# Kernel tuning notes

Hardware: AMD Instinct MI355X
Metric: run time of the kernel (lower is better)

## Reference

```python
import jax, jax.numpy as jnp
import numpy as np

NUM_LAYERS = 3
CHANNELS = 8
IN_CHANNELS = 8
MASK_FEAT_STRIDE = 8
MASK_OUT_STRIDE = 4
FACTOR = MASK_FEAT_STRIDE // MASK_OUT_STRIDE  # 2

# param split sizes (weights first, then biases), matching parse_dynamic_params
W0 = (IN_CHANNELS + 2) * CHANNELS  # 80
W1 = CHANNELS * CHANNELS           # 64
W2 = CHANNELS * 1                  # 8
B0 = CHANNELS
B1 = CHANNELS
B2 = 1
NUM_GEN_PARAMS = W0 + W1 + W2 + B0 + B1 + B2  # 169


def compute_locations(h, w, stride):
    # matches adet.utils.comm.compute_locations: centers of stride-cells, (x, y)
    sx = jnp.arange(w, dtype=jnp.float32) * stride + stride // 2
    sy = jnp.arange(h, dtype=jnp.float32) * stride + stride // 2
    yy, xx = jnp.meshgrid(sy, sx, indexing='ij')
    return jnp.stack([xx.reshape(-1), yy.reshape(-1)], axis=1)  # [H*W, 2]


def _interp_axis_align(x, out_size, axis):
    # 1D bilinear with align_corners=True along `axis`
    in_size = x.shape[axis]
    pos = jnp.arange(out_size, dtype=jnp.float32) * ((in_size - 1) / (out_size - 1))
    i0 = jnp.floor(pos).astype(jnp.int32)
    i1 = jnp.minimum(i0 + 1, in_size - 1)
    w1 = (pos - i0.astype(jnp.float32)).astype(x.dtype)
    shape = [1] * x.ndim
    shape[axis] = out_size
    w1 = w1.reshape(shape)
    x0 = jnp.take(x, i0, axis=axis)
    x1 = jnp.take(x, i1, axis=axis)
    return x0 * (1 - w1) + x1 * w1


def aligned_bilinear(t, factor):
    # matches adet.utils.comm.aligned_bilinear
    if factor == 1:
        return t
    h, w = t.shape[2], t.shape[3]
    t = jnp.pad(t, ((0, 0), (0, 0), (0, 1), (0, 1)), mode='edge')
    oh, ow = factor * h + 1, factor * w + 1
    t = _interp_axis_align(t, oh, 2)
    t = _interp_axis_align(t, ow, 3)
    pad = factor // 2
    t = jnp.pad(t, ((0, 0), (0, 0), (pad, 0), (pad, 0)), mode='edge')
    return t[:, :, :oh - 1, :ow - 1]  # [N, C, factor*h, factor*w]


def setup_inputs() -> dict:
    key = jax.random.key(0)
    k1, k2, k3, k4, k5 = jax.random.split(key, 5)
    N, H, W = 2, 128, 192
    n_inst = 128
    mask_feats = jax.random.normal(k1, (N, IN_CHANNELS, H, W), dtype=jnp.float32)
    mask_head_params = jax.random.normal(k2, (n_inst, NUM_GEN_PARAMS), dtype=jnp.float32) * 0.1
    instance_locations = jax.random.uniform(k3, (n_inst, 2), dtype=jnp.float32) * 1024.0
    sizes_of_interest = jnp.array([64.0, 128.0, 256.0, 512.0, 1e8, 2e8], dtype=jnp.float32)
    im_inds = jax.random.randint(k4, (n_inst,), 0, N, dtype=jnp.int32)
    fpn_levels = jax.random.randint(k5, (n_inst,), 0, 5, dtype=jnp.int32)
    return {
        'mask_feats': mask_feats,
        'mask_head_params': mask_head_params,
        'instance_locations': instance_locations,
        'sizes_of_interest': sizes_of_interest,
        'im_inds': im_inds,
        'fpn_levels': fpn_levels,
    }


def reference(mask_feats, mask_head_params, instance_locations, sizes_of_interest, im_inds, fpn_levels):
    N, C, H, W = mask_feats.shape
    n = mask_head_params.shape[0]
    HW = H * W

    locs = compute_locations(H, W, MASK_FEAT_STRIDE)                 # [HW, 2]
    rel = instance_locations[:, None, :] - locs[None, :, :]          # [n, HW, 2]
    rel = jnp.transpose(rel, (0, 2, 1))                              # [n, 2, HW]
    soi = sizes_of_interest[fpn_levels]                              # [n]
    rel = rel / soi[:, None, None]

    feats = mask_feats[im_inds].reshape(n, C, HW)                    # gather per-instance image feats
    x = jnp.concatenate([rel, feats], axis=1)                        # [n, C+2, HW]

    p = mask_head_params
    w0 = p[:, :W0].reshape(n, CHANNELS, IN_CHANNELS + 2)
    w1 = p[:, W0:W0 + W1].reshape(n, CHANNELS, CHANNELS)
    w2 = p[:, W0 + W1:W0 + W1 + W2].reshape(n, 1, CHANNELS)
    off = W0 + W1 + W2
    b0 = p[:, off:off + B0]
    b1 = p[:, off + B0:off + B0 + B1]
    b2 = p[:, off + B0 + B1:off + B0 + B1 + B2]

    # per-instance dynamic 1x1-conv MLP (grouped conv == batched matmul)
    x = jax.nn.relu(jnp.einsum('noi,nip->nop', w0, x) + b0[:, :, None])
    x = jax.nn.relu(jnp.einsum('noi,nip->nop', w1, x) + b1[:, :, None])
    x = jnp.einsum('noi,nip->nop', w2, x) + b2[:, :, None]           # [n, 1, HW]

    mask_logits = x.reshape(n, 1, H, W)
    return aligned_bilinear(mask_logits, FACTOR)                     # [n, 1, 2H, 2W]
```

## Files before the change

kernel.cpp:

```cpp
#include <hip/hip_runtime.h>
#include <hip/hip_bf16.h>

#define NUM_INST 128
#define H_ 128
#define W_ 192
#define HW_ (H_ * W_)
#define OH_ 256
#define OW_ 384
#define NPAR 169

typedef float v2f __attribute__((ext_vector_type(2)));

static __device__ __forceinline__ float bf2f(unsigned short u) {
    union { unsigned int i; float f; } v;
    v.i = ((unsigned int)u) << 16;
    return v.f;
}
static __device__ __forceinline__ float hi2f(unsigned int u) {
    union { unsigned int i; float f; } v;
    v.i = u & 0xFFFF0000u;
    return v.f;
}
static __device__ __forceinline__ float lo2f(unsigned int u) {
    union { unsigned int i; float f; } v;
    v.i = u << 16;
    return v.f;
}
static __device__ __forceinline__ unsigned int f2bf(float f) {
    unsigned int u = __float_as_uint(f);
    return (u + 0x7fffu + ((u >> 16) & 1u)) >> 16;
}
static __device__ __forceinline__ v2f pkfma(v2f a, v2f b, v2f c) {
    return __builtin_elementwise_fma(a, b, c);
}
static __device__ __forceinline__ v2f pkrelu(v2f a) {
    const v2f z = {0.0f, 0.0f};
    return __builtin_elementwise_max(a, z);
}

__global__ __launch_bounds__(256) void fused_maskhead(
    const void* __restrict__ mf_v,
    const void* __restrict__ par_v,
    const void* __restrict__ loc_v,
    const void* __restrict__ soi_v,
    const int*  __restrict__ im_inds,
    const int*  __restrict__ fpn,
    void*       __restrict__ out_v)
{
    const int tid  = threadIdx.x;
    const int inst = blockIdx.y;
    const int r0   = blockIdx.x * 8;

    const bool f32in = (*(const unsigned int*)soi_v) == 0x42800000u;

    __shared__ __align__(16) float w0p[8][12];
    __shared__ __align__(16) float w1p[8][12];
    __shared__ __align__(16) float w2p[12];
    __shared__ __align__(16) float b1p[8];
    __shared__ float Lt[9][W_ + 2];

    auto ldpar = [&](int k) -> float {
        return f32in ? ((const float*)par_v)[inst * NPAR + k]
                     : bf2f(((const unsigned short*)par_v)[inst * NPAR + k]);
    };

    if (tid < 96) {
        const int o = tid / 12, i = tid - o * 12;
        float v = 0.0f;
        if (i < 10) v = ldpar(o * 10 + i);
        else if (i == 10) v = ldpar(152 + o);
        w0p[o][i] = v;
    } else if (tid < 192) {
        const int t = tid - 96, o = t / 12, i = t - o * 12;
        float v = 0.0f;
        if (i < 8) v = ldpar(80 + o * 8 + i);
        else if (i == 8) v = ldpar(160 + o);
        w1p[o][i] = v;
    } else if (tid < 204) {
        const int t = tid - 192;
        float v = 0.0f;
        if (t < 8) v = ldpar(144 + t);
        else if (t == 8) v = ldpar(168);
        w2p[t] = v;
    } else if (tid < 212) {
        b1p[tid - 204] = ldpar(160 + tid - 204);
    }

    float lx, ly, soi;
    const int lvl = fpn[inst];
    if (f32in) {
        lx  = ((const float*)loc_v)[inst * 2 + 0];
        ly  = ((const float*)loc_v)[inst * 2 + 1];
        soi = ((const float*)soi_v)[lvl];
    } else {
        lx  = bf2f(((const unsigned short*)loc_v)[inst * 2 + 0]);
        ly  = bf2f(((const unsigned short*)loc_v)[inst * 2 + 1]);
        soi = bf2f(((const unsigned short*)soi_v)[lvl]);
    }
    const float invs = 1.0f / soi;
    const size_t fo  = (size_t)im_inds[inst] * 8 * HW_;

    __syncthreads();

    auto do_group = [&](int g) {
        const int j  = g / 48;
        const int c0 = (g - j * 48) * 4;
        int rr = r0 - 1 + j; if (rr < 0) rr = 0;
        const int poff = rr * W_ + c0;

        const float dy  = (ly - (float)(rr * 8 + 4)) * invs;
        const float dx0 = (lx - (float)(c0 * 8 + 4)) * invs;
        const float st  = -8.0f * invs;

        v2f xA[9], xB[9];
        xA[0] = (v2f){dx0, dx0 + st};
        xB[0] = (v2f){dx0 + 2.0f * st, dx0 + 3.0f * st};
        if (f32in) {
            const float* fb = (const float*)mf_v + fo + poff;
#pragma unroll
            for (int ch = 0; ch < 8; ch++) {
                float4 f = *(const float4*)(fb + ch * HW_);
                xA[1 + ch] = (v2f){f.x, f.y};
                xB[1 + ch] = (v2f){f.z, f.w};
            }
        } else {
            const unsigned short* fb = (const unsigned short*)mf_v + fo + poff;
#pragma unroll
            for (int ch = 0; ch < 8; ch++) {
                uint2 f = *(const uint2*)(fb + ch * HW_);
                xA[1 + ch] = (v2f){lo2f(f.x), hi2f(f.x)};
                xB[1 + ch] = (v2f){lo2f(f.y), hi2f(f.y)};
            }
        }

        v2f h1A[8], h1B[8];
#pragma unroll
        for (int o = 0; o < 8; o++) {
            const float4 qa = *(const float4*)&w0p[o][0];
            const float4 qb = *(const float4*)&w0p[o][4];
            const float4 qc = *(const float4*)&w0p[o][8];
            const float wl[9] = {qa.x, qa.z, qa.w, qb.x, qb.y,
                                 qb.z, qb.w, qc.x, qc.y};
            const float t = fmaf(qa.y, dy, qc.z);
            v2f a01 = (v2f){t, t}, a23 = (v2f){t, t};
#pragma unroll
            for (int i = 0; i < 9; i++) {
                const v2f ws = (v2f){wl[i], wl[i]};
                a01 = pkfma(ws, xA[i], a01);
                a23 = pkfma(ws, xB[i], a23);
            }
            h1A[o] = pkrelu(a01);
            h1B[o] = pkrelu(a23);
        }

        const float4 bqa = *(const float4*)&b1p[0];
        const float4 bqb = *(const float4*)&b1p[4];
        const float b1r[8] = {bqa.x, bqa.y, bqa.z, bqa.w,
                              bqb.x, bqb.y, bqb.z, bqb.w};
        v2f h2A[8], h2B[8];
#pragma unroll
        for (int o = 0; o < 8; o++) {
            const float4 qa = *(const float4*)&w1p[o][0];
            const float4 qb = *(const float4*)&w1p[o][4];
            const float wl[8] = {qa.x, qa.y, qa.z, qa.w,
                                 qb.x, qb.y, qb.z, qb.w};
            const float b = b1r[o];
            v2f a01 = (v2f){b, b}, a23 = (v2f){b, b};
#pragma unroll
            for (int i = 0; i < 8; i++) {
                const v2f ws = (v2f){wl[i], wl[i]};
                a01 = pkfma(ws, h1A[i], a01);
                a23 = pkfma(ws, h1B[i], a23);
            }
            h2A[o] = pkrelu(a01);
            h2B[o] = pkrelu(a23);
        }

        const float4 qa = *(const float4*)&w2p[0];
        const float4 qb = *(const float4*)&w2p[4];
        const float wl[8] = {qa.x, qa.y, qa.z, qa.w, qb.x, qb.y, qb.z, qb.w};
        const float b2 = w2p[8];
        v2f oA = (v2f){b2, b2}, oB = (v2f){b2, b2};
#pragma unroll
        for (int i = 0; i < 8; i++) {
            const v2f ws = (v2f){wl[i], wl[i]};
            oA = pkfma(ws, h2A[i], oA);
            oB = pkfma(ws, h2B[i], oB);
        }

        *(v2f*)&Lt[j][c0]     = oA;
        *(v2f*)&Lt[j][c0 + 2] = oB;
    };

    do_group(tid);
    if (tid < 176) do_group(tid + 256);

    __syncthreads();

    for (int q = tid; q < 1536; q += 256) {
        const int rl = q / 192;
        const int c  = q - rl * 192;
        const int r  = r0 + rl;
        const int cm = c ? c - 1 : 0;

        const float a = Lt[rl][cm],     b = Lt[rl][c];
        const float d = Lt[rl + 1][cm], e = Lt[rl + 1][c];

        const float v00 = 0.25f * (a + b + d + e);
        const float v01 = 0.5f  * (b + e);
        const float v10 = 0.5f  * (d + e);
        const float v11 = e;

        const size_t base = ((size_t)inst * OH_ + 2 * r) * (size_t)OW_ + 2 * c;
        if (f32in) {
            float* of = (float*)out_v;
            *(float2*)(of + base)       = make_float2(v00, v01);
            *(float2*)(of + base + OW_) = make_float2(v10, v11);
        } else {
            unsigned int* ob = (unsigned int*)out_v;
            ob[base >> 1]         = f2bf(v00) | (f2bf(v01) << 16);
            ob[(base + OW_) >> 1] = f2bf(v10) | (f2bf(v11) << 16);
        }
    }
}

extern "C" void kernel_launch(void* const* d_in, const int* in_sizes, int n_in,
                              void* d_out, int out_size, void* d_ws, size_t ws_size,
                              hipStream_t stream) {
    (void)in_sizes; (void)n_in; (void)d_ws; (void)ws_size; (void)out_size;
    dim3 grid(H_ / 8, NUM_INST);
    fused_maskhead<<<grid, 256, 0, stream>>>(d_in[0], d_in[1], d_in[2], d_in[3],
                                             (const int*)d_in[4],
                                             (const int*)d_in[5], d_out);
}
```

Before: 118.3 us.

## Split fused mask head into separate MLP and upsample kernels via workspace

Replaces the single fused kernel, which recomputed a halo row per 8-row tile and staged logits in shared memory, with two kernels. The first runs the per-instance MLP over 2 pixels per thread and writes fp32 logits to a global workspace. The second reads the logits back and does the 2x aligned bilinear upsample with wider stores. This removes the halo recompute and the intra-block barriers, at the cost of a roughly 12.6 MB workspace round trip and a second launch.

```diff
diff --git a/kernel.cpp b/kernel.cpp
--- a/kernel.cpp
+++ b/kernel.cpp
@@ -38,18 +38,17 @@
     return __builtin_elementwise_max(a, z);
 }
 
-__global__ __launch_bounds__(256) void fused_maskhead(
+__global__ __launch_bounds__(256, 4) void mlp_kernel(
     const void* __restrict__ mf_v,
     const void* __restrict__ par_v,
     const void* __restrict__ loc_v,
     const void* __restrict__ soi_v,
     const int*  __restrict__ im_inds,
     const int*  __restrict__ fpn,
-    void*       __restrict__ out_v)
+    float*      __restrict__ logits)
 {
     const int tid  = threadIdx.x;
     const int inst = blockIdx.y;
-    const int r0   = blockIdx.x * 8;
 
     const bool f32in = (*(const unsigned int*)soi_v) == 0x42800000u;
 
@@ -57,7 +56,6 @@
     __shared__ __align__(16) float w1p[8][12];
     __shared__ __align__(16) float w2p[12];
     __shared__ __align__(16) float b1p[8];
-    __shared__ float Lt[9][W_ + 2];
 
     auto ldpar = [&](int k) -> float {
         return f32in ? ((const float*)par_v)[inst * NPAR + k]
@@ -102,134 +100,136 @@
 
     __syncthreads();
 
-    auto do_group = [&](int g) {
-        const int j  = g / 48;
-        const int c0 = (g - j * 48) * 4;
-        int rr = r0 - 1 + j; if (rr < 0) rr = 0;
-        const int poff = rr * W_ + c0;
-
-        const float dy  = (ly - (float)(rr * 8 + 4)) * invs;
-        const float dx0 = (lx - (float)(c0 * 8 + 4)) * invs;
-        const float st  = -8.0f * invs;
-
-        v2f xA[9], xB[9];
-        xA[0] = (v2f){dx0, dx0 + st};
-        xB[0] = (v2f){dx0 + 2.0f * st, dx0 + 3.0f * st};
-        if (f32in) {
-            const float* fb = (const float*)mf_v + fo + poff;
-#pragma unroll
-            for (int ch = 0; ch < 8; ch++) {
-                float4 f = *(const float4*)(fb + ch * HW_);
-                xA[1 + ch] = (v2f){f.x, f.y};
-                xB[1 + ch] = (v2f){f.z, f.w};
-            }
-        } else {
-            const unsigned short* fb = (const unsigned short*)mf_v + fo + poff;
-#pragma unroll
-            for (int ch = 0; ch < 8; ch++) {
-                uint2 f = *(const uint2*)(fb + ch * HW_);
-                xA[1 + ch] = (v2f){lo2f(f.x), hi2f(f.x)};
-                xB[1 + ch] = (v2f){lo2f(f.y), hi2f(f.y)};
-            }
+    const int p0 = (blockIdx.x * 256 + tid) * 2;
+    const int r  = p0 / W_;
+    const int c0 = p0 - r * W_;
+
+    const float dy  = (ly - (float)(r * 8 + 4)) * invs;
+    const float dx0 = (lx - (float)(c0 * 8 + 4)) * invs;
+    const float st  = -8.0f * invs;
+
+    v2f x[9];
+    x[0] = (v2f){dx0, dx0 + st};
+    if (f32in) {
+        const float* fb = (const float*)mf_v + fo + (r * W_ + c0);
+#pragma unroll
+        for (int ch = 0; ch < 8; ch++) {
+            float2 f = *(const float2*)(fb + ch * HW_);
+            x[1 + ch] = (v2f){f.x, f.y};
         }
-
-        v2f h1A[8], h1B[8];
-#pragma unroll
-        for (int o = 0; o < 8; o++) {
-            const float4 qa = *(const float4*)&w0p[o][0];
-            const float4 qb = *(const float4*)&w0p[o][4];
-            const float4 qc = *(const float4*)&w0p[o][8];
-            const float wl[9] = {qa.x, qa.z, qa.w, qb.x, qb.y,
-                                 qb.z, qb.w, qc.x, qc.y};
-            const float t = fmaf(qa.y, dy, qc.z);
-            v2f a01 = (v2f){t, t}, a23 = (v2f){t, t};
-#pragma unroll
-            for (int i = 0; i < 9; i++) {
-                const v2f ws = (v2f){wl[i], wl[i]};
-                a01 = pkfma(ws, xA[i], a01);
-                a23 = pkfma(ws, xB[i], a23);
-            }
-            h1A[o] = pkrelu(a01);
-            h1B[o] = pkrelu(a23);
+    } else {
+        const unsigned short* fb = (const unsigned short*)mf_v + fo + (r * W_ + c0);
+#pragma unroll
+        for (int ch = 0; ch < 8; ch++) {
+            unsigned int f = *(const unsigned int*)(fb + ch * HW_);
+            x[1 + ch] = (v2f){lo2f(f), hi2f(f)};
         }
-
-        const float4 bqa = *(const float4*)&b1p[0];
-        const float4 bqb = *(const float4*)&b1p[4];
-        const float b1r[8] = {bqa.x, bqa.y, bqa.z, bqa.w,
-                              bqb.x, bqb.y, bqb.z, bqb.w};
-        v2f h2A[8], h2B[8];
-#pragma unroll
-        for (int o = 0; o < 8; o++) {
-            const float4 qa = *(const float4*)&w1p[o][0];
-            const float4 qb = *(const float4*)&w1p[o][4];
-            const float wl[8] = {qa.x, qa.y, qa.z, qa.w,
-                                 qb.x, qb.y, qb.z, qb.w};
-            const float b = b1r[o];
-            v2f a01 = (v2f){b, b}, a23 = (v2f){b, b};
-#pragma unroll
-            for (int i = 0; i < 8; i++) {
-                const v2f ws = (v2f){wl[i], wl[i]};
-                a01 = pkfma(ws, h1A[i], a01);
-                a23 = pkfma(ws, h1B[i], a23);
-            }
-            h2A[o] = pkrelu(a01);
-            h2B[o] = pkrelu(a23);
-        }
-
-        const float4 qa = *(const float4*)&w2p[0];
-        const float4 qb = *(const float4*)&w2p[4];
+    }
+
+    v2f h1[8];
+#pragma unroll
+    for (int o = 0; o < 8; o++) {
+        const float4 qa = *(const float4*)&w0p[o][0];
+        const float4 qb = *(const float4*)&w0p[o][4];
+        const float4 qc = *(const float4*)&w0p[o][8];
+        const float wl[9] = {qa.x, qa.z, qa.w, qb.x, qb.y,
+                             qb.z, qb.w, qc.x, qc.y};
+        const float t = fmaf(qa.y, dy, qc.z);
+        v2f a = (v2f){t, t};
+#pragma unroll
+        for (int i = 0; i < 9; i++)
+            a = pkfma((v2f){wl[i], wl[i]}, x[i], a);
+        h1[o] = pkrelu(a);
+    }
+
+    const float4 bqa = *(const float4*)&b1p[0];
+    const float4 bqb = *(const float4*)&b1p[4];
+    const float b1r[8] = {bqa.x, bqa.y, bqa.z, bqa.w,
+                          bqb.x, bqb.y, bqb.z, bqb.w};
+    v2f h2[8];
+#pragma unroll
+    for (int o = 0; o < 8; o++) {
+        const float4 qa = *(const float4*)&w1p[o][0];
+        const float4 qb = *(const float4*)&w1p[o][4];
         const float wl[8] = {qa.x, qa.y, qa.z, qa.w, qb.x, qb.y, qb.z, qb.w};
-        const float b2 = w2p[8];
-        v2f oA = (v2f){b2, b2}, oB = (v2f){b2, b2};
-#pragma unroll
-        for (int i = 0; i < 8; i++) {
-            const v2f ws = (v2f){wl[i], wl[i]};
-            oA = pkfma(ws, h2A[i], oA);
-            oB = pkfma(ws, h2B[i], oB);
-        }
-
-        *(v2f*)&Lt[j][c0]     = oA;
-        *(v2f*)&Lt[j][c0 + 2] = oB;
-    };
-
-    do_group(tid);
-    if (tid < 176) do_group(tid + 256);
-
-    __syncthreads();
-
-    for (int q = tid; q < 1536; q += 256) {
-        const int rl = q / 192;
-        const int c  = q - rl * 192;
-        const int r  = r0 + rl;
-        const int cm = c ? c - 1 : 0;
-
-        const float a = Lt[rl][cm],     b = Lt[rl][c];
-        const float d = Lt[rl + 1][cm], e = Lt[rl + 1][c];
-
-        const float v00 = 0.25f * (a + b + d + e);
-        const float v01 = 0.5f  * (b + e);
-        const float v10 = 0.5f  * (d + e);
-        const float v11 = e;
-
-        const size_t base = ((size_t)inst * OH_ + 2 * r) * (size_t)OW_ + 2 * c;
-        if (f32in) {
-            float* of = (float*)out_v;
-            *(float2*)(of + base)       = make_float2(v00, v01);
-            *(float2*)(of + base + OW_) = make_float2(v10, v11);
-        } else {
-            unsigned int* ob = (unsigned int*)out_v;
-            ob[base >> 1]         = f2bf(v00) | (f2bf(v01) << 16);
-            ob[(base + OW_) >> 1] = f2bf(v10) | (f2bf(v11) << 16);
-        }
+        v2f a = (v2f){b1r[o], b1r[o]};
+#pragma unroll
+        for (int i = 0; i < 8; i++)
+            a = pkfma((v2f){wl[i], wl[i]}, h1[i], a);
+        h2[o] = pkrelu(a);
+    }
+
+    const float4 qa = *(const float4*)&w2p[0];
+    const float4 qb = *(const float4*)&w2p[4];
+    const float wl[8] = {qa.x, qa.y, qa.z, qa.w, qb.x, qb.y, qb.z, qb.w};
+    v2f o2 = (v2f){w2p[8], w2p[8]};
+#pragma unroll
+    for (int i = 0; i < 8; i++)
+        o2 = pkfma((v2f){wl[i], wl[i]}, h2[i], o2);
+
+    *(v2f*)(logits + (size_t)inst * HW_ + p0) = o2;
+}
+
+__global__ __launch_bounds__(256) void upsample_kernel(
+    const float* __restrict__ logits,
+    const void*  __restrict__ soi_v,
+    void*        __restrict__ out_v)
+{
+    const bool f32in = (*(const unsigned int*)soi_v) == 0x42800000u;
+
+    const int inst = blockIdx.y;
+    const int t  = blockIdx.x * 256 + threadIdx.x;
+    const int r  = t / 96;
+    const int cp = t - r * 96;
+    const int c  = 2 * cp;
+    const int cm = c ? c - 1 : 0;
+    const int rm = r ? r - 1 : 0;
+
+    const float* L  = logits + (size_t)inst * HW_;
+    const float* rU = L + rm * W_;
+    const float* rD = L + r * W_;
+
+    const float  aL = rU[cm];
+    const float2 a01 = *(const float2*)(rU + c);
+    const float  dL = rD[cm];
+    const float2 d01 = *(const float2*)(rD + c);
+
+    const float v00 = 0.25f * (aL + a01.x + dL + d01.x);
+    const float v01 = 0.5f  * (a01.x + d01.x);
+    const float v10 = 0.5f  * (dL + d01.x);
+    const float v11 = d01.x;
+    const float u00 = 0.25f * (a01.x + a01.y + d01.x + d01.y);
+    const float u01 = 0.5f  * (a01.y + d01.y);
+    const float u10 = 0.5f  * (d01.x + d01.y);
+    const float u11 = d01.y;
+
+    const size_t base = ((size_t)inst * OH_ + 2 * r) * (size_t)OW_ + 2 * c;
+    if (f32in) {
+        float* of = (float*)out_v;
+        *(float4*)(of + base)       = make_float4(v00, v01, u00, u01);
+        *(float4*)(of + base + OW_) = make_float4(v10, v11, u10, u11);
+    } else {
+        unsigned int* ob = (unsigned int*)out_v;
+        const size_t i0 = base >> 1;
+        ob[i0]     = f2bf(v00) | (f2bf(v01) << 16);
+        ob[i0 + 1] = f2bf(u00) | (f2bf(u01) << 16);
+        const size_t i1 = (base + OW_) >> 1;
+        ob[i1]     = f2bf(v10) | (f2bf(v11) << 16);
+        ob[i1 + 1] = f2bf(u10) | (f2bf(u11) << 16);
     }
 }
 
 extern "C" void kernel_launch(void* const* d_in, const int* in_sizes, int n_in,
                               void* d_out, int out_size, void* d_ws, size_t ws_size,
                               hipStream_t stream) {
-    (void)in_sizes; (void)n_in; (void)d_ws; (void)ws_size; (void)out_size;
-    dim3 grid(H_ / 8, NUM_INST);
-    fused_maskhead<<<grid, 256, 0, stream>>>(d_in[0], d_in[1], d_in[2], d_in[3],
-                                             (const int*)d_in[4],
-                                             (const int*)d_in[5], d_out);
-}
+    (void)in_sizes; (void)n_in; (void)ws_size; (void)out_size;
+    float* logits = (float*)d_ws;
+
+    dim3 g1(HW_ / (256 * 2), NUM_INST);
+    mlp_kernel<<<g1, 256, 0, stream>>>(d_in[0], d_in[1], d_in[2], d_in[3],
+                                       (const int*)d_in[4], (const int*)d_in[5],
+                                       logits);
+
+    dim3 g2((H_ * (W_ / 2)) / 256, NUM_INST);
+    upsample_kernel<<<g2, 256, 0, stream>>>(logits, d_in[3], d_out);
+}
```

Result: faster. 103.3 us (-12.7%).
